# Performance work log

Hardware: AMD Instinct MI355X
Metric: run time of the kernel (lower is better)

## Reference

```python
import jax, jax.numpy as jnp
import numpy as np
import math

B, LQ, LK = 4, 512, 512
D_MODEL, NHEAD, NLABELS = 512, 8, 8
D_Q = D_MODEL // NHEAD


def setup_inputs() -> dict:
    key = jax.random.key(0)
    ks = jax.random.split(key, 12)
    xavier = lambda k, shape: jax.random.uniform(
        k, shape, jnp.float32,
        -math.sqrt(6.0 / (shape[0] + shape[1])), math.sqrt(6.0 / (shape[0] + shape[1])))
    return {
        "q": jax.random.normal(ks[0], (B, LQ, D_MODEL), jnp.float32),
        "k": jax.random.normal(ks[1], (B, LK, D_MODEL), jnp.float32),
        "edge_mask": jax.random.randint(ks[2], (B, LQ, LK, NLABELS), 0, 2).astype(jnp.float32),
        "padding_mask": jax.random.randint(ks[3], (B, LQ, LK), 0, 2).astype(jnp.float32),
        "w_q_w": xavier(ks[4], (D_MODEL, D_MODEL)),
        "w_q_b": jnp.zeros((D_MODEL,), jnp.float32),
        "w_k": xavier(ks[5], (D_MODEL, D_MODEL)),
        "w_v": xavier(ks[6], (D_MODEL, D_MODEL)),
        "w_h_w": xavier(ks[7], (D_MODEL, D_MODEL)),
        "w_h_b": jnp.zeros((D_MODEL,), jnp.float32),
        "b_ks": xavier(ks[8], (NLABELS, D_Q)),
        "b_vs": xavier(ks[9], (NLABELS, D_Q)),
    }


def reference(q, k, edge_mask, padding_mask, w_q_w, w_q_b, w_k, w_v, w_h_w, w_h_b, b_ks, b_vs):
    sz_b, len_q, _ = q.shape
    len_k = k.shape[1]
    temp = np.power(D_Q, 0.5).astype(np.float32)

    # projections -> (nhead, B, L, d_q), matching torch permute(2,0,1,3)
    query = (q @ w_q_w.T + w_q_b).reshape(sz_b, len_q, NHEAD, D_Q).transpose(2, 0, 1, 3)
    key = (k @ w_k.T).reshape(sz_b, len_k, NHEAD, D_Q).transpose(2, 0, 1, 3)
    value = (k @ w_v.T).reshape(sz_b, len_k, NHEAD, D_Q).transpose(2, 0, 1, 3)

    # content scores + relation-bias scores
    qk = jnp.einsum('hbqd,hbkd->hbqk', query, key)
    key_rel = jnp.einsum('bqkl,ld->bqkd', edge_mask, b_ks)      # (B,Lq,Lk,d_q)
    qkr = jnp.einsum('hbqd,bqkd->hbqk', query, key_rel)
    output_attention_weights = (qk + qkr) / temp                # pre-mask, as returned by torch

    # mask where no edge label AND padding_mask==1
    relation_mask = (edge_mask.sum(-1) + (1.0 - padding_mask)) == 0  # (B,Lq,Lk)
    rm = relation_mask[None, :, :, :]                                # broadcast over heads
    attn = jnp.where(rm, -jnp.inf, output_attention_weights)
    attn = jax.nn.softmax(attn, axis=-1)
    attn = jnp.where(rm, 0.0, attn)

    # value aggregation: content + relation values
    qv = jnp.einsum('hbqk,hbkd->hbqd', attn, value)
    val_rel = jnp.einsum('bqkl,ld->bqkd', edge_mask, b_vs)
    qvr = jnp.einsum('hbqk,bqkd->hbqd', attn, val_rel)

    out = (qv + qvr).transpose(1, 2, 0, 3).reshape(sz_b, len_q, D_MODEL)
    out = out @ w_h_w.T + w_h_b
    return out, output_attention_weights.reshape(NHEAD * sz_b, len_q, len_k)
```

## Files before the change

### kernel.cpp

```cpp
#include <hip/hip_runtime.h>
#include <math.h>

#define NB 4
#define LQ 512
#define LK 512
#define DM 512
#define NH 8
#define DQ 64
#define NL 8
#define QT 32
#define PSTR 520

typedef short bf16x8 __attribute__((ext_vector_type(8)));
typedef _Float16 f16x8 __attribute__((ext_vector_type(8)));
typedef _Float16 f16x2 __attribute__((ext_vector_type(2)));
typedef float f32x4 __attribute__((ext_vector_type(4)));

__device__ __forceinline__ unsigned short f2bf(float x) {
    unsigned u = __float_as_uint(x);
    u += 0x7fff + ((u >> 16) & 1);
    return (unsigned short)(u >> 16);
}
__device__ __forceinline__ float bf2f(unsigned x) {
    return __uint_as_float(x << 16);
}
__device__ __forceinline__ unsigned short f2h(float x) {
    _Float16 h = (_Float16)x;
    return __builtin_bit_cast(unsigned short, h);
}
__device__ __forceinline__ void gld16(const void* g, void* l) {
    __builtin_amdgcn_global_load_lds(
        (const __attribute__((address_space(1))) void*)g,
        (__attribute__((address_space(3))) void*)l, 16, 0, 0);
}

__global__ __launch_bounds__(256) void prep_kernel(
        const float* __restrict__ q,  const float* __restrict__ k,
        const float* __restrict__ wq, const float* __restrict__ wk,
        const float* __restrict__ wv, const float* __restrict__ wh,
        const float* __restrict__ em, const float* __restrict__ pad,
        unsigned short* __restrict__ qb,  unsigned short* __restrict__ kb,
        unsigned short* __restrict__ wqb, unsigned short* __restrict__ wkb,
        unsigned short* __restrict__ wvb, unsigned short* __restrict__ whb,
        unsigned short* __restrict__ Pk) {
    const int tid = threadIdx.x;
    const int y = blockIdx.y;
    if (y < 6) {
        const float* s; unsigned short* d; int n;
        switch (y) {
            case 0: s = q;  d = qb;  n = NB * LQ * DM; break;
            case 1: s = k;  d = kb;  n = NB * LK * DM; break;
            case 2: s = wq; d = wqb; n = DM * DM; break;
            case 3: s = wk; d = wkb; n = DM * DM; break;
            case 4: s = wv; d = wvb; n = DM * DM; break;
            default: s = wh; d = whb; n = DM * DM; break;
        }
        const int i = blockIdx.x * 256 + tid;
        if (i * 8 >= n) return;
        const float4* sv = (const float4*)s;
        const float4 a = sv[2 * (size_t)i], b = sv[2 * (size_t)i + 1];
        uint4 o;
        o.x = (unsigned)f2bf(a.x) | ((unsigned)f2bf(a.y) << 16);
        o.y = (unsigned)f2bf(a.z) | ((unsigned)f2bf(a.w) << 16);
        o.z = (unsigned)f2bf(b.x) | ((unsigned)f2bf(b.y) << 16);
        o.w = (unsigned)f2bf(b.z) | ((unsigned)f2bf(b.w) << 16);
        *(uint4*)(d + (size_t)i * 8) = o;
    } else {
        if (blockIdx.x >= 512) return;
        const int row = blockIdx.x * 4 + (tid >> 6);
        const int k0 = (tid & 63) * 8;
        const float* eb = em + ((size_t)row * LK + k0) * NL;
        const float4 pv0 = *(const float4*)(pad + (size_t)row * LK + k0);
        const float4 pv1 = *(const float4*)(pad + (size_t)row * LK + k0 + 4);
        const float pv[8] = {pv0.x, pv0.y, pv0.z, pv0.w, pv1.x, pv1.y, pv1.z, pv1.w};
        unsigned short outv[8];
#pragma unroll
        for (int kk = 0; kk < 8; ++kk) {
            const float4 v0 = *(const float4*)(eb + kk * 8);
            const float4 v1 = *(const float4*)(eb + kk * 8 + 4);
            unsigned b_ = 0;
            b_ |= (v0.x != 0.f) << 0; b_ |= (v0.y != 0.f) << 1;
            b_ |= (v0.z != 0.f) << 2; b_ |= (v0.w != 0.f) << 3;
            b_ |= (v1.x != 0.f) << 4; b_ |= (v1.y != 0.f) << 5;
            b_ |= (v1.z != 0.f) << 6; b_ |= (v1.w != 0.f) << 7;
            b_ |= (pv[kk] != 0.f) << 8;
            outv[kk] = (unsigned short)b_;
        }
        uint4 o;
        o.x = (unsigned)outv[0] | ((unsigned)outv[1] << 16);
        o.y = (unsigned)outv[2] | ((unsigned)outv[3] << 16);
        o.z = (unsigned)outv[4] | ((unsigned)outv[5] << 16);
        o.w = (unsigned)outv[6] | ((unsigned)outv[7] << 16);
        *(uint4*)(Pk + (size_t)row * LK + k0) = o;
    }
}

__device__ __forceinline__ void gemm64core(const unsigned short* __restrict__ Ag, int lda,
                                           const unsigned short* __restrict__ Bg, int ldb,
                                           int K, short* As, short* Bs,
                                           f32x4 (&acc)[2][2]) {
    const int tid = threadIdx.x;
    const int wave = tid >> 6, lane = tid & 63;
    const int quad = lane >> 4, l16 = lane & 15;
    const int wr = wave >> 1, wc = wave & 1;
    for (int k0 = 0; k0 < K; k0 += 32) {
        __syncthreads();
        gld16(Ag + (size_t)(tid >> 2) * lda + k0 + (tid & 3) * 8, (char*)As + wave * 1024);
        gld16(Bg + (size_t)(tid >> 2) * ldb + k0 + (tid & 3) * 8, (char*)Bs + wave * 1024);
        __syncthreads();
        bf16x8 af[2], bf[2];
#pragma unroll
        for (int i = 0; i < 2; ++i)
            af[i] = *(const bf16x8*)&As[(wr * 32 + i * 16 + l16) * 32 + quad * 8];
#pragma unroll
        for (int j = 0; j < 2; ++j)
            bf[j] = *(const bf16x8*)&Bs[(wc * 32 + j * 16 + l16) * 32 + quad * 8];
#pragma unroll
        for (int i = 0; i < 2; ++i)
#pragma unroll
            for (int j = 0; j < 2; ++j)
                acc[i][j] = __builtin_amdgcn_mfma_f32_16x16x32_bf16(af[i], bf[j], acc[i][j], 0, 0, 0);
    }
}

__global__ __launch_bounds__(256) void proj_all(const unsigned short* __restrict__ qb,
                                                const unsigned short* __restrict__ kb,
                                                const unsigned short* __restrict__ wqb,
                                                const unsigned short* __restrict__ wkb,
                                                const unsigned short* __restrict__ wvb,
                                                const float* __restrict__ w_q_b,
                                                unsigned short* __restrict__ Qp,
                                                unsigned short* __restrict__ Kp,
                                                unsigned short* __restrict__ Vt) {
    __shared__ __align__(16) short As[64 * 32];
    __shared__ __align__(16) short Bs[64 * 32];
    const unsigned short* A; const unsigned short* W; const float* bias;
    unsigned short* C; int mode;
    switch (blockIdx.z) {
        case 0:  A = qb; W = wqb; bias = w_q_b;  C = Qp; mode = 0; break;
        case 1:  A = kb; W = wkb; bias = nullptr; C = Kp; mode = 0; break;
        default: A = kb; W = wvb; bias = nullptr; C = Vt; mode = 1; break;
    }
    f32x4 acc[2][2];
    const f32x4 zz = {0.f, 0.f, 0.f, 0.f};
#pragma unroll
    for (int i = 0; i < 2; ++i)
#pragma unroll
        for (int j = 0; j < 2; ++j) acc[i][j] = zz;
    const int m0 = blockIdx.x * 64, n0 = blockIdx.y * 64;
    gemm64core(A + (size_t)m0 * DM, DM, W + (size_t)n0 * DM, DM, DM, As, Bs, acc);
    const int tid = threadIdx.x, wave = tid >> 6, lane = tid & 63;
    const int quad = lane >> 4, l16 = lane & 15;
    const int wr = wave >> 1, wc = wave & 1;
#pragma unroll
    for (int i = 0; i < 2; ++i)
#pragma unroll
        for (int r = 0; r < 4; ++r) {
            const int gm = m0 + wr * 32 + i * 16 + quad * 4 + r;
#pragma unroll
            for (int j = 0; j < 2; ++j) {
                const int gn = n0 + wc * 32 + j * 16 + l16;
                float v = acc[i][j][r];
                if (bias) v += bias[gn];
                if (mode == 0) C[(size_t)gm * DM + gn] = f2bf(v);
                else C[(size_t)(gm >> 9) * (DM * LK) + (size_t)gn * LK + (gm & 511)] = f2h(v);
            }
        }
}

__global__ __launch_bounds__(512, 4) void attn_fused(
        const unsigned short* __restrict__ Qp,
        const unsigned short* __restrict__ Kp,
        const unsigned short* __restrict__ Vt,
        const unsigned short* __restrict__ Pk,
        const float* __restrict__ b_ks,
        const float* __restrict__ b_vs,
        float* __restrict__ weights,
        unsigned short* __restrict__ Hb) {
    __shared__ __align__(16) short Qs[QT * 64];
    __shared__ __align__(16) short Kc[128 * 64];
    __shared__ __align__(16) short Ps[QT * PSTR];
    __shared__ float svS[QT * NL];
    __shared__ float lutS[QT * 32];
    __shared__ float tS[QT * NL];
    __shared__ float redA[QT * 8];
    __shared__ float redB[QT * 8];

    const int tid = threadIdx.x, wave = tid >> 6, lane = tid & 63;
    const int quad = lane >> 4, l16 = lane & 15;
    const int q0 = blockIdx.x * QT;
    const int z = blockIdx.y, h = z >> 2, b = z & 3;

    if (tid < 256) {
        const int row = tid >> 3, ch = tid & 7;
        gld16(Qp + (size_t)(b * LQ + q0 + row) * DM + h * DQ + ((ch ^ (row & 7)) * 8),
              (char*)Qs + wave * 1024);
    }

    {
        const int row = tid >> 4, l = (tid >> 1) & 7, half = tid & 1;
        const unsigned short* qrow = Qp + (size_t)(b * LQ + q0 + row) * DM + h * DQ + half * 32;
        const float* bk = b_ks + l * DQ + half * 32;
        float s = 0.f;
#pragma unroll
        for (int d0 = 0; d0 < 32; d0 += 8) {
            const bf16x8 qv = *(const bf16x8*)&qrow[d0];
#pragma unroll
            for (int j = 0; j < 8; ++j)
                s = fmaf(bf2f((unsigned short)qv[j]), bk[d0 + j], s);
        }
        s += __shfl_xor(s, 1, 64);
        if (half == 0) svS[row * 8 + l] = s;
    }

    f32x4 acc[4][2];
    const f32x4 zz = {0.f, 0.f, 0.f, 0.f};
#pragma unroll
    for (int c = 0; c < 4; ++c) { acc[c][0] = zz; acc[c][1] = zz; }
    bf16x8 qf[2][2];

    for (int c = 0; c < 4; ++c) {
#pragma unroll
        for (int it = 0; it < 2; ++it) {
            const int e = it * 512 + tid;
            const int kr = e >> 3, ch = e & 7;
            gld16(Kp + (size_t)(b * LK + c * 128 + kr) * DM + h * DQ + ((ch ^ (kr & 7)) * 8),
                  (char*)Kc + it * 8192 + wave * 1024);
        }
        __syncthreads();
        if (c == 0) {
#pragma unroll
            for (int i = 0; i < 2; ++i)
#pragma unroll
                for (int kdi = 0; kdi < 2; ++kdi)
                    qf[i][kdi] = *(const bf16x8*)&Qs[(i * 16 + l16) * 64
                                                     + (((kdi * 4) + quad) ^ (l16 & 7)) * 8];
        }
#pragma unroll
        for (int kdi = 0; kdi < 2; ++kdi) {
            const int krow = wave * 16 + l16;
            const int kch = (kdi * 4 + quad) ^ (krow & 7);
            const bf16x8 bfv = *(const bf16x8*)&Kc[krow * 64 + kch * 8];
#pragma unroll
            for (int i = 0; i < 2; ++i)
                acc[c][i] = __builtin_amdgcn_mfma_f32_16x16x32_bf16(qf[i][kdi], bfv, acc[c][i], 0, 0, 0);
        }
        if (c == 0) {
            for (int e = tid; e < QT * 32; e += 512) {
                const int row = e >> 5, idx = e & 31;
                const float* s = &svS[row * 8 + ((idx & 16) ? 4 : 0)];
                float v = 0.f;
                v += (idx & 1) ? s[0] : 0.f;
                v += (idx & 2) ? s[1] : 0.f;
                v += (idx & 4) ? s[2] : 0.f;
                v += (idx & 8) ? s[3] : 0.f;
                lutS[e] = v;
            }
        }
        __syncthreads();
    }

#pragma unroll
    for (int it = 0; it < 2; ++it) {
        const int e = it * 512 + tid;
        const int dd = e >> 4, ch = e & 15;
        gld16(Vt + (size_t)(b * DM + h * DQ + dd) * LK + ((ch ^ (dd & 15)) * 8),
              (char*)Kc + it * 8192 + wave * 1024);
    }

#pragma unroll
    for (int i = 0; i < 2; ++i)
#pragma unroll
        for (int r = 0; r < 4; ++r) {
            const int row = i * 16 + quad * 4 + r;
            const int gq = q0 + row;
            const float* lrow = &lutS[row * 32];
            const unsigned short* prow = Pk + (size_t)(b * LQ + gq) * LK;
            float* wrow = weights + ((size_t)z * LQ + gq) * LK;
            float pm = -__builtin_inff();
#pragma unroll
            for (int c = 0; c < 4; ++c) {
                const int col = c * 128 + wave * 16 + l16;
                const unsigned w_ = prow[col];
                const float rel = lrow[w_ & 15u] + lrow[16 + ((w_ >> 4) & 15u)];
                const float wv = (acc[c][i][r] + rel) * 0.125f;
                wrow[col] = wv;
                const float m = ((w_ & 0x1FFu) == 0x100u) ? -__builtin_inff() : wv;
                acc[c][i][r] = m;
                pm = fmaxf(pm, m);
            }
#pragma unroll
            for (int o = 1; o < 16; o <<= 1) pm = fmaxf(pm, __shfl_xor(pm, o, 64));
            float ps = 0.f;
#pragma unroll
            for (int c = 0; c < 4; ++c) {
                const float e = __expf(acc[c][i][r] - pm);
                acc[c][i][r] = e;
                ps += e;
            }
#pragma unroll
            for (int o = 1; o < 16; o <<= 1) ps += __shfl_xor(ps, o, 64);
            if (l16 == 0) { redA[row * 8 + wave] = pm; redB[row * 8 + wave] = ps; }
        }
    __syncthreads();

#pragma unroll
    for (int i = 0; i < 2; ++i)
#pragma unroll
        for (int r = 0; r < 4; ++r) {
            const int row = i * 16 + quad * 4 + r;
            const f32x4 pa = *(const f32x4*)&redA[row * 8];
            const f32x4 pb = *(const f32x4*)&redA[row * 8 + 4];
            const f32x4 sa = *(const f32x4*)&redB[row * 8];
            const f32x4 sb = *(const f32x4*)&redB[row * 8 + 4];
            const float M = fmaxf(fmaxf(fmaxf(pa[0], pa[1]), fmaxf(pa[2], pa[3])),
                                  fmaxf(fmaxf(pb[0], pb[1]), fmaxf(pb[2], pb[3])));
            const float S = sa[0] * __expf(pa[0] - M) + sa[1] * __expf(pa[1] - M)
                          + sa[2] * __expf(pa[2] - M) + sa[3] * __expf(pa[3] - M)
                          + sb[0] * __expf(pb[0] - M) + sb[1] * __expf(pb[1] - M)
                          + sb[2] * __expf(pb[2] - M) + sb[3] * __expf(pb[3] - M);
            const float own = redA[row * 8 + wave];
            const float alpha = __expf(own - M) / S;
#pragma unroll
            for (int c = 0; c < 4; ++c) {
                const int col = c * 128 + wave * 16 + l16;
                Ps[row * PSTR + col] = (short)f2h(acc[c][i][r] * alpha);
            }
        }
    __syncthreads();

    {
        const int row = tid >> 4, l = (tid >> 1) & 7, half = tid & 1;
        const uint4* pw = (const uint4*)(Pk + (size_t)(b * LQ + q0 + row) * LK + half * 256);
        const uint4* aw = (const uint4*)&Ps[row * PSTR + half * 256];
        float tv = 0.f;
#pragma unroll 4
        for (int kk = 0; kk < 32; ++kk) {
            const uint4 wb = pw[kk];
            const uint4 av = aw[kk];
            const unsigned w4[4] = {wb.x, wb.y, wb.z, wb.w};
            const unsigned a4[4] = {av.x, av.y, av.z, av.w};
            f16x2 hacc = {(_Float16)0.f, (_Float16)0.f};
#pragma unroll
            for (int u = 0; u < 4; ++u) {
                const unsigned bits = (w4[u] >> l) & 0x10001u;
                const unsigned msk = bits * 0x3c00u;
                hacc += __builtin_bit_cast(f16x2, a4[u]) * __builtin_bit_cast(f16x2, msk);
            }
            tv += (float)hacc[0] + (float)hacc[1];
        }
        tv += __shfl_xor(tv, 1, 64);
        if (half == 0) tS[row * 8 + l] = tv;
    }

    f32x4 oacc = zz;
    const int mi = wave & 1, ni = wave >> 1;
    for (int vc = 0; vc < 4; ++vc) {
        if (vc > 0) {
            __syncthreads();
#pragma unroll
            for (int it = 0; it < 2; ++it) {
                const int e = it * 512 + tid;
                const int dd = e >> 4, ch = e & 15;
                gld16(Vt + (size_t)(b * DM + h * DQ + dd) * LK + vc * 128 + ((ch ^ (dd & 15)) * 8),
                      (char*)Kc + it * 8192 + wave * 1024);
            }
            __syncthreads();
        }
#pragma unroll
        for (int kd = 0; kd < 128; kd += 32) {
            const int vrow = ni * 16 + l16;
            const int vch = ((kd >> 3) + quad) ^ (vrow & 15);
            const f16x8 afv = *(const f16x8*)&Ps[(mi * 16 + l16) * PSTR + vc * 128 + kd + quad * 8];
            const f16x8 bfv = *(const f16x8*)&Kc[vrow * 128 + vch * 8];
            oacc = __builtin_amdgcn_mfma_f32_16x16x32_f16(afv, bfv, oacc, 0, 0, 0);
        }
    }

    const int gd = ni * 16 + l16;
    float bvv[NL];
#pragma unroll
    for (int l = 0; l < NL; ++l) bvv[l] = b_vs[l * DQ + gd];
#pragma unroll
    for (int r = 0; r < 4; ++r) {
        const int row = mi * 16 + quad * 4 + r;
        const float* tp = &tS[row * 8];
        float o = oacc[r];
#pragma unroll
        for (int l = 0; l < NL; ++l) o = fmaf(tp[l], bvv[l], o);
        Hb[(size_t)(b * LQ + q0 + row) * DM + h * DQ + gd] = f2bf(o);
    }
}

__global__ __launch_bounds__(256) void outproj_mfma(const unsigned short* __restrict__ Hb,
                                                    const unsigned short* __restrict__ whb,
                                                    const float* __restrict__ bias,
                                                    float* __restrict__ C) {
    __shared__ __align__(16) short As[64 * 32];
    __shared__ __align__(16) short Bs[64 * 32];
    f32x4 acc[2][2];
    const f32x4 zz = {0.f, 0.f, 0.f, 0.f};
#pragma unroll
    for (int i = 0; i < 2; ++i)
#pragma unroll
        for (int j = 0; j < 2; ++j) acc[i][j] = zz;
    const int m0 = blockIdx.x * 64, n0 = blockIdx.y * 64;
    gemm64core(Hb + (size_t)m0 * DM, DM, whb + (size_t)n0 * DM, DM, DM, As, Bs, acc);
    const int tid = threadIdx.x, wave = tid >> 6, lane = tid & 63;
    const int quad = lane >> 4, l16 = lane & 15;
    const int wr = wave >> 1, wc = wave & 1;
#pragma unroll
    for (int i = 0; i < 2; ++i)
#pragma unroll
        for (int r = 0; r < 4; ++r) {
            const int gm = m0 + wr * 32 + i * 16 + quad * 4 + r;
#pragma unroll
            for (int j = 0; j < 2; ++j) {
                const int gn = n0 + wc * 32 + j * 16 + l16;
                C[(size_t)gm * DM + gn] = acc[i][j][r] + bias[gn];
            }
        }
}

extern "C" void kernel_launch(void* const* d_in, const int* in_sizes, int n_in,
                              void* d_out, int out_size, void* d_ws, size_t ws_size,
                              hipStream_t stream) {
    const float* q     = (const float*)d_in[0];
    const float* k     = (const float*)d_in[1];
    const float* em    = (const float*)d_in[2];
    const float* pad   = (const float*)d_in[3];
    const float* w_q_w = (const float*)d_in[4];
    const float* w_q_b = (const float*)d_in[5];
    const float* w_k   = (const float*)d_in[6];
    const float* w_v   = (const float*)d_in[7];
    const float* w_h_w = (const float*)d_in[8];
    const float* w_h_b = (const float*)d_in[9];
    const float* b_ks  = (const float*)d_in[10];
    const float* b_vs  = (const float*)d_in[11];

    float* out     = (float*)d_out;
    float* weights = out + (size_t)NB * LQ * DM;

    char* ws = (char*)d_ws;
    unsigned short* qb  = (unsigned short*)(ws + 0);
    unsigned short* kb  = (unsigned short*)(ws + 2097152);
    unsigned short* wqb = (unsigned short*)(ws + 4194304);
    unsigned short* wkb = (unsigned short*)(ws + 4718592);
    unsigned short* wvb = (unsigned short*)(ws + 5242880);
    unsigned short* whb = (unsigned short*)(ws + 5767168);
    unsigned short* Qp  = (unsigned short*)(ws + 6291456);
    unsigned short* Kp  = (unsigned short*)(ws + 8388608);
    unsigned short* Vt  = (unsigned short*)(ws + 10485760);
    unsigned short* Hb  = (unsigned short*)(ws + 12582912);
    unsigned short* Pk  = (unsigned short*)(ws + 14680064);

    prep_kernel<<<dim3(1024, 7), 256, 0, stream>>>(q, k, w_q_w, w_k, w_v, w_h_w,
                                                   em, pad, qb, kb, wqb, wkb, wvb, whb, Pk);
    proj_all<<<dim3(32, 8, 3), 256, 0, stream>>>(qb, kb, wqb, wkb, wvb, w_q_b, Qp, Kp, Vt);
    attn_fused<<<dim3(LQ / QT, 32), 512, 0, stream>>>(Qp, Kp, Vt, Pk, b_ks, b_vs, weights, Hb);
    outproj_mfma<<<dim3(32, 8), 256, 0, stream>>>(Hb, whb, w_h_b, out);
}
```

Baseline: 168.1 us.

## Double-buffer LDS staging in GEMM and attention K/V loops with async prefetch

The projection and output GEMM core and the attention kernel's K and V chunk loads now use two LDS buffers. The next tile is issued via global_load_lds while the current one is consumed, with explicit vmcnt/lgkmcnt waits and raw barriers instead of paired __syncthreads. This is meant to hide global load latency behind MFMA work. It doubles LDS use for K/V staging, which can cut occupancy in the attention kernel, and the hand-placed waits are fragile. The prep kernel grid is also trimmed to the number of blocks that actually do work.

Result: no change. 166.6 us (-0.9%).

```diff
diff --git a/kernel.cpp b/kernel.cpp
--- a/kernel.cpp
+++ b/kernel.cpp
@@ -33,6 +33,12 @@
         (const __attribute__((address_space(1))) void*)g,
         (__attribute__((address_space(3))) void*)l, 16, 0, 0);
 }
+
+#define WAITVM(N) asm volatile("s_waitcnt vmcnt(" #N ")" ::: "memory")
+#define LGKM0()   asm volatile("s_waitcnt lgkmcnt(0)" ::: "memory")
+#define BARR()    do { asm volatile("" ::: "memory"); \
+                       __builtin_amdgcn_s_barrier();  \
+                       asm volatile("" ::: "memory"); } while (0)
 
 __global__ __launch_bounds__(256) void prep_kernel(
         const float* __restrict__ q,  const float* __restrict__ k,
@@ -66,7 +72,6 @@
         o.w = (unsigned)f2bf(b.z) | ((unsigned)f2bf(b.w) << 16);
         *(uint4*)(d + (size_t)i * 8) = o;
     } else {
-        if (blockIdx.x >= 512) return;
         const int row = blockIdx.x * 4 + (tid >> 6);
         const int k0 = (tid & 63) * 8;
         const float* eb = em + ((size_t)row * LK + k0) * NL;
@@ -97,29 +102,42 @@
 
 __device__ __forceinline__ void gemm64core(const unsigned short* __restrict__ Ag, int lda,
                                            const unsigned short* __restrict__ Bg, int ldb,
-                                           int K, short* As, short* Bs,
+                                           short* As, short* Bs,
                                            f32x4 (&acc)[2][2]) {
     const int tid = threadIdx.x;
     const int wave = tid >> 6, lane = tid & 63;
     const int quad = lane >> 4, l16 = lane & 15;
     const int wr = wave >> 1, wc = wave & 1;
-    for (int k0 = 0; k0 < K; k0 += 32) {
-        __syncthreads();
-        gld16(Ag + (size_t)(tid >> 2) * lda + k0 + (tid & 3) * 8, (char*)As + wave * 1024);
-        gld16(Bg + (size_t)(tid >> 2) * ldb + k0 + (tid & 3) * 8, (char*)Bs + wave * 1024);
-        __syncthreads();
+    const int r_ = tid >> 2, c_ = (tid & 3) * 8;
+    const unsigned short* Ar = Ag + (size_t)r_ * lda + c_;
+    const unsigned short* Br = Bg + (size_t)r_ * ldb + c_;
+    gld16(Ar, (char*)As + wave * 1024);
+    gld16(Br, (char*)Bs + wave * 1024);
+#pragma unroll
+    for (int s = 0; s < 16; ++s) {
+        if (s < 15) {
+            const int nb = (s + 1) & 1;
+            gld16(Ar + (s + 1) * 32, (char*)As + nb * 4096 + wave * 1024);
+            gld16(Br + (s + 1) * 32, (char*)Bs + nb * 4096 + wave * 1024);
+            WAITVM(2);
+        } else {
+            WAITVM(0);
+        }
+        BARR();
+        const int cb = s & 1;
         bf16x8 af[2], bf[2];
 #pragma unroll
         for (int i = 0; i < 2; ++i)
-            af[i] = *(const bf16x8*)&As[(wr * 32 + i * 16 + l16) * 32 + quad * 8];
+            af[i] = *(const bf16x8*)&As[cb * 2048 + (wr * 32 + i * 16 + l16) * 32 + quad * 8];
 #pragma unroll
         for (int j = 0; j < 2; ++j)
-            bf[j] = *(const bf16x8*)&Bs[(wc * 32 + j * 16 + l16) * 32 + quad * 8];
+            bf[j] = *(const bf16x8*)&Bs[cb * 2048 + (wc * 32 + j * 16 + l16) * 32 + quad * 8];
 #pragma unroll
         for (int i = 0; i < 2; ++i)
 #pragma unroll
             for (int j = 0; j < 2; ++j)
                 acc[i][j] = __builtin_amdgcn_mfma_f32_16x16x32_bf16(af[i], bf[j], acc[i][j], 0, 0, 0);
+        BARR();
     }
 }
 
@@ -132,8 +150,8 @@
                                                 unsigned short* __restrict__ Qp,
                                                 unsigned short* __restrict__ Kp,
                                                 unsigned short* __restrict__ Vt) {
-    __shared__ __align__(16) short As[64 * 32];
-    __shared__ __align__(16) short Bs[64 * 32];
+    __shared__ __align__(16) short As[2][64 * 32];
+    __shared__ __align__(16) short Bs[2][64 * 32];
     const unsigned short* A; const unsigned short* W; const float* bias;
     unsigned short* C; int mode;
     switch (blockIdx.z) {
@@ -148,7 +166,7 @@
 #pragma unroll
         for (int j = 0; j < 2; ++j) acc[i][j] = zz;
     const int m0 = blockIdx.x * 64, n0 = blockIdx.y * 64;
-    gemm64core(A + (size_t)m0 * DM, DM, W + (size_t)n0 * DM, DM, DM, As, Bs, acc);
+    gemm64core(A + (size_t)m0 * DM, DM, W + (size_t)n0 * DM, DM, &As[0][0], &Bs[0][0], acc);
     const int tid = threadIdx.x, wave = tid >> 6, lane = tid & 63;
     const int quad = lane >> 4, l16 = lane & 15;
     const int wr = wave >> 1, wc = wave & 1;
@@ -167,6 +185,49 @@
             }
         }
 }
+
+#define STAGE_K(c, hb) do {                                                       \
+    _Pragma("unroll")                                                             \
+    for (int it_ = 0; it_ < 2; ++it_) {                                           \
+        const int e_ = it_ * 512 + tid;                                           \
+        const int kr_ = e_ >> 3, ch_ = e_ & 7;                                    \
+        gld16(Kp + (size_t)(b * LK + (c) * 128 + kr_) * DM + h * DQ               \
+                  + ((ch_ ^ (kr_ & 7)) * 8),                                      \
+              (char*)&Kc[hb][0] + it_ * 8192 + wave * 1024);                      \
+    } } while (0)
+
+#define STAGE_V(vc, hb) do {                                                      \
+    _Pragma("unroll")                                                             \
+    for (int it_ = 0; it_ < 2; ++it_) {                                           \
+        const int e_ = it_ * 512 + tid;                                           \
+        const int dd_ = e_ >> 4, ch_ = e_ & 15;                                   \
+        gld16(Vt + (size_t)(b * DM + h * DQ + dd_) * LK + (vc) * 128              \
+                  + ((ch_ ^ (dd_ & 15)) * 8),                                     \
+              (char*)&Kc[hb][0] + it_ * 8192 + wave * 1024);                      \
+    } } while (0)
+
+#define COMPUTE_K(c, hb) do {                                                     \
+    _Pragma("unroll")                                                             \
+    for (int kdi_ = 0; kdi_ < 2; ++kdi_) {                                        \
+        const int krow_ = wave * 16 + l16;                                        \
+        const int kch_ = (kdi_ * 4 + quad) ^ (krow_ & 7);                         \
+        const bf16x8 bfv_ = *(const bf16x8*)&Kc[hb][krow_ * 64 + kch_ * 8];       \
+        acc[c][0] = __builtin_amdgcn_mfma_f32_16x16x32_bf16(qf[0][kdi_], bfv_,    \
+                                                            acc[c][0], 0, 0, 0); \
+        acc[c][1] = __builtin_amdgcn_mfma_f32_16x16x32_bf16(qf[1][kdi_], bfv_,    \
+                                                            acc[c][1], 0, 0, 0); \
+    } } while (0)
+
+#define COMPUTE_V(vc, hb) do {                                                    \
+    _Pragma("unroll")                                                             \
+    for (int kd_ = 0; kd_ < 128; kd_ += 32) {                                     \
+        const int vrow_ = ni * 16 + l16;                                          \
+        const int vch_ = ((kd_ >> 3) + quad) ^ (vrow_ & 15);                      \
+        const f16x8 afv_ = *(const f16x8*)&Ps[(mi * 16 + l16) * PSTR              \
+                                              + (vc) * 128 + kd_ + quad * 8];     \
+        const f16x8 bfv_ = *(const f16x8*)&Kc[hb][vrow_ * 128 + vch_ * 8];        \
+        oacc = __builtin_amdgcn_mfma_f32_16x16x32_f16(afv_, bfv_, oacc, 0, 0, 0); \
+    } } while (0)
 
 __global__ __launch_bounds__(512, 4) void attn_fused(
         const unsigned short* __restrict__ Qp,
@@ -178,7 +239,7 @@
         float* __restrict__ weights,
         unsigned short* __restrict__ Hb) {
     __shared__ __align__(16) short Qs[QT * 64];
-    __shared__ __align__(16) short Kc[128 * 64];
+    __shared__ __align__(16) short Kc[2][128 * 64];
     __shared__ __align__(16) short Ps[QT * PSTR];
     __shared__ float svS[QT * NL];
     __shared__ float lutS[QT * 32];
@@ -191,26 +252,32 @@
     const int q0 = blockIdx.x * QT;
     const int z = blockIdx.y, h = z >> 2, b = z & 3;
 
+    const int srow = tid >> 4, sl = (tid >> 1) & 7, shalf = tid & 1;
+    bf16x8 sq[4];
+    {
+        const unsigned short* qrow = Qp + (size_t)(b * LQ + q0 + srow) * DM + h * DQ + shalf * 32;
+#pragma unroll
+        for (int d0 = 0; d0 < 4; ++d0) sq[d0] = *(const bf16x8*)&qrow[d0 * 8];
+    }
+
     if (tid < 256) {
         const int row = tid >> 3, ch = tid & 7;
         gld16(Qp + (size_t)(b * LQ + q0 + row) * DM + h * DQ + ((ch ^ (row & 7)) * 8),
               (char*)Qs + wave * 1024);
     }
+    STAGE_K(0, 0);
+    STAGE_K(1, 1);
 
     {
-        const int row = tid >> 4, l = (tid >> 1) & 7, half = tid & 1;
-        const unsigned short* qrow = Qp + (size_t)(b * LQ + q0 + row) * DM + h * DQ + half * 32;
-        const float* bk = b_ks + l * DQ + half * 32;
+        const float* bk = b_ks + sl * DQ + shalf * 32;
         float s = 0.f;
 #pragma unroll
-        for (int d0 = 0; d0 < 32; d0 += 8) {
-            const bf16x8 qv = *(const bf16x8*)&qrow[d0];
+        for (int d0 = 0; d0 < 4; ++d0)
 #pragma unroll
             for (int j = 0; j < 8; ++j)
-                s = fmaf(bf2f((unsigned short)qv[j]), bk[d0 + j], s);
-        }
+                s = fmaf(bf2f((unsigned short)sq[d0][j]), bk[d0 * 8 + j], s);
         s += __shfl_xor(s, 1, 64);
-        if (half == 0) svS[row * 8 + l] = s;
+        if (shalf == 0) svS[srow * 8 + sl] = s;
     }
 
     f32x4 acc[4][2];
@@ -219,54 +286,40 @@
     for (int c = 0; c < 4; ++c) { acc[c][0] = zz; acc[c][1] = zz; }
     bf16x8 qf[2][2];
 
-    for (int c = 0; c < 4; ++c) {
-#pragma unroll
-        for (int it = 0; it < 2; ++it) {
-            const int e = it * 512 + tid;
-            const int kr = e >> 3, ch = e & 7;
-            gld16(Kp + (size_t)(b * LK + c * 128 + kr) * DM + h * DQ + ((ch ^ (kr & 7)) * 8),
-                  (char*)Kc + it * 8192 + wave * 1024);
-        }
-        __syncthreads();
-        if (c == 0) {
-#pragma unroll
-            for (int i = 0; i < 2; ++i)
-#pragma unroll
-                for (int kdi = 0; kdi < 2; ++kdi)
-                    qf[i][kdi] = *(const bf16x8*)&Qs[(i * 16 + l16) * 64
-                                                     + (((kdi * 4) + quad) ^ (l16 & 7)) * 8];
-        }
-#pragma unroll
-        for (int kdi = 0; kdi < 2; ++kdi) {
-            const int krow = wave * 16 + l16;
-            const int kch = (kdi * 4 + quad) ^ (krow & 7);
-            const bf16x8 bfv = *(const bf16x8*)&Kc[krow * 64 + kch * 8];
-#pragma unroll
-            for (int i = 0; i < 2; ++i)
-                acc[c][i] = __builtin_amdgcn_mfma_f32_16x16x32_bf16(qf[i][kdi], bfv, acc[c][i], 0, 0, 0);
-        }
-        if (c == 0) {
-            for (int e = tid; e < QT * 32; e += 512) {
-                const int row = e >> 5, idx = e & 31;
-                const float* s = &svS[row * 8 + ((idx & 16) ? 4 : 0)];
-                float v = 0.f;
-                v += (idx & 1) ? s[0] : 0.f;
-                v += (idx & 2) ? s[1] : 0.f;
-                v += (idx & 4) ? s[2] : 0.f;
-                v += (idx & 8) ? s[3] : 0.f;
-                lutS[e] = v;
-            }
-        }
-        __syncthreads();
-    }
-
-#pragma unroll
-    for (int it = 0; it < 2; ++it) {
-        const int e = it * 512 + tid;
-        const int dd = e >> 4, ch = e & 15;
-        gld16(Vt + (size_t)(b * DM + h * DQ + dd) * LK + ((ch ^ (dd & 15)) * 8),
-              (char*)Kc + it * 8192 + wave * 1024);
-    }
+    WAITVM(2); LGKM0(); BARR();
+#pragma unroll
+    for (int i = 0; i < 2; ++i)
+#pragma unroll
+        for (int kdi = 0; kdi < 2; ++kdi)
+            qf[i][kdi] = *(const bf16x8*)&Qs[(i * 16 + l16) * 64
+                                             + (((kdi * 4) + quad) ^ (l16 & 7)) * 8];
+#pragma unroll
+    for (int e2 = 0; e2 < 2; ++e2) {
+        const int e = e2 * 512 + tid;
+        const int row = e >> 5, idx = e & 31;
+        const float* sp = &svS[row * 8 + ((idx & 16) ? 4 : 0)];
+        float v = 0.f;
+        v += (idx & 1) ? sp[0] : 0.f;
+        v += (idx & 2) ? sp[1] : 0.f;
+        v += (idx & 4) ? sp[2] : 0.f;
+        v += (idx & 8) ? sp[3] : 0.f;
+        lutS[e] = v;
+    }
+    COMPUTE_K(0, 0);
+    LGKM0(); BARR();
+    STAGE_K(2, 0);
+    WAITVM(2); LGKM0(); BARR();
+    COMPUTE_K(1, 1);
+    LGKM0(); BARR();
+    STAGE_K(3, 1);
+    WAITVM(2); LGKM0(); BARR();
+    COMPUTE_K(2, 0);
+    LGKM0(); BARR();
+    STAGE_V(0, 0);
+    WAITVM(2); LGKM0(); BARR();
+    COMPUTE_K(3, 1);
+    LGKM0(); BARR();
+    STAGE_V(1, 1);
 
 #pragma unroll
     for (int i = 0; i < 2; ++i)
@@ -302,7 +355,7 @@
             for (int o = 1; o < 16; o <<= 1) ps += __shfl_xor(ps, o, 64);
             if (l16 == 0) { redA[row * 8 + wave] = pm; redB[row * 8 + wave] = ps; }
         }
-    __syncthreads();
+    LGKM0(); BARR();
 
 #pragma unroll
     for (int i = 0; i < 2; ++i)
@@ -327,7 +380,7 @@
                 Ps[row * PSTR + col] = (short)f2h(acc[c][i][r] * alpha);
             }
         }
-    __syncthreads();
+    LGKM0(); BARR();
 
     {
         const int row = tid >> 4, l = (tid >> 1) & 7, half = tid & 1;
@@ -355,27 +408,18 @@
 
     f32x4 oacc = zz;
     const int mi = wave & 1, ni = wave >> 1;
-    for (int vc = 0; vc < 4; ++vc) {
-        if (vc > 0) {
-            __syncthreads();
-#pragma unroll
-            for (int it = 0; it < 2; ++it) {
-                const int e = it * 512 + tid;
-                const int dd = e >> 4, ch = e & 15;
-                gld16(Vt + (size_t)(b * DM + h * DQ + dd) * LK + vc * 128 + ((ch ^ (dd & 15)) * 8),
-                      (char*)Kc + it * 8192 + wave * 1024);
-            }
-            __syncthreads();
-        }
-#pragma unroll
-        for (int kd = 0; kd < 128; kd += 32) {
-            const int vrow = ni * 16 + l16;
-            const int vch = ((kd >> 3) + quad) ^ (vrow & 15);
-            const f16x8 afv = *(const f16x8*)&Ps[(mi * 16 + l16) * PSTR + vc * 128 + kd + quad * 8];
-            const f16x8 bfv = *(const f16x8*)&Kc[vrow * 128 + vch * 8];
-            oacc = __builtin_amdgcn_mfma_f32_16x16x32_f16(afv, bfv, oacc, 0, 0, 0);
-        }
-    }
+    WAITVM(0); LGKM0(); BARR();
+    COMPUTE_V(0, 0);
+    BARR();
+    STAGE_V(2, 0);
+    WAITVM(2); LGKM0(); BARR();
+    COMPUTE_V(1, 1);
+    BARR();
+    STAGE_V(3, 1);
+    WAITVM(2); LGKM0(); BARR();
+    COMPUTE_V(2, 0);
+    WAITVM(0); LGKM0(); BARR();
+    COMPUTE_V(3, 1);
 
     const int gd = ni * 16 + l16;
     float bvv[NL];
@@ -396,8 +440,8 @@
                                                     const unsigned short* __restrict__ whb,
                                                     const float* __restrict__ bias,
                                                     float* __restrict__ C) {
-    __shared__ __align__(16) short As[64 * 32];
-    __shared__ __align__(16) short Bs[64 * 32];
+    __shared__ __align__(16) short As[2][64 * 32];
+    __shared__ __align__(16) short Bs[2][64 * 32];
     f32x4 acc[2][2];
     const f32x4 zz = {0.f, 0.f, 0.f, 0.f};
 #pragma unroll
@@ -405,7 +449,7 @@
 #pragma unroll
         for (int j = 0; j < 2; ++j) acc[i][j] = zz;
     const int m0 = blockIdx.x * 64, n0 = blockIdx.y * 64;
-    gemm64core(Hb + (size_t)m0 * DM, DM, whb + (size_t)n0 * DM, DM, DM, As, Bs, acc);
+    gemm64core(Hb + (size_t)m0 * DM, DM, whb + (size_t)n0 * DM, DM, &As[0][0], &Bs[0][0], acc);
     const int tid = threadIdx.x, wave = tid >> 6, lane = tid & 63;
     const int quad = lane >> 4, l16 = lane & 15;
     const int wr = wave >> 1, wc = wave & 1;
@@ -454,8 +498,8 @@
     unsigned short* Hb  = (unsigned short*)(ws + 12582912);
     unsigned short* Pk  = (unsigned short*)(ws + 14680064);
 
-    prep_kernel<<<dim3(1024, 7), 256, 0, stream>>>(q, k, w_q_w, w_k, w_v, w_h_w,
-                                                   em, pad, qb, kb, wqb, wkb, wvb, whb, Pk);
+    prep_kernel<<<dim3(512, 7), 256, 0, stream>>>(q, k, w_q_w, w_k, w_v, w_h_w,
+                                                  em, pad, qb, kb, wqb, wkb, wvb, whb, Pk);
     proj_all<<<dim3(32, 8, 3), 256, 0, stream>>>(qb, kb, wqb, wkb, wvb, w_q_b, Qp, Kp, Vt);
     attn_fused<<<dim3(LQ / QT, 32), 512, 0, stream>>>(Qp, Kp, Vt, Pk, b_ks, b_vs, weights, Hb);
     outproj_mfma<<<dim3(32, 8), 256, 0, stream>>>(Hb, whb, w_h_b, out);
```
